# Kernel tuning notes

Measured on AMD Instinct MI355X. Metric: run time of the kernel, lower is better.

Reference implementation:

```python
import jax, jax.numpy as jnp
import numpy as np

HIDDEN = 2048
HEAD_DIM = 128
GROUPS = 8
HEADS = HIDDEN // HEAD_DIM          # 16
HPG = HEADS // GROUPS               # heads per group = 2


def setup_inputs() -> dict:
    key = jax.random.key(0)
    ks = jax.random.split(key, 9)
    b, sl, sk = 2, 2048, 2048
    s = 0.02
    return {
        "q": jax.random.normal(ks[0], (b, sl, HIDDEN), jnp.float32),
        "k": jax.random.normal(ks[1], (b, sk, HIDDEN), jnp.float32),
        "v": jax.random.normal(ks[2], (b, sk, HIDDEN), jnp.float32),
        "Wq": jax.random.normal(ks[3], (HIDDEN, HIDDEN), jnp.float32) * s,
        "bq": jax.random.normal(ks[4], (HIDDEN,), jnp.float32) * s,
        "Wk": jax.random.normal(ks[5], (HIDDEN, HEAD_DIM * GROUPS), jnp.float32) * s,
        "bk": jax.random.normal(ks[6], (HEAD_DIM * GROUPS,), jnp.float32) * s,
        "Wv": jax.random.normal(ks[7], (HIDDEN, HEAD_DIM * GROUPS), jnp.float32) * s,
        "bv": jax.random.normal(ks[8], (HEAD_DIM * GROUPS,), jnp.float32) * s,
    }


def reference(q, k, v, Wq, bq, Wk, bk, Wv, bv):
    b, sl, _ = q.shape
    sk = k.shape[1]
    qp = q @ Wq + bq                                   # [b, sl, hidden]
    kp = k @ Wk + bk                                   # [b, sk, G*d]
    vp = v @ Wv + bv                                   # [b, sk, G*d]
    # head h = g*HPG + j uses group g, matching torch repeat_interleave on dim=1
    qh = qp.reshape(b, sl, GROUPS, HPG, HEAD_DIM).transpose(0, 2, 3, 1, 4)  # [b,G,hpg,sl,d]
    kh = kp.reshape(b, sk, GROUPS, HEAD_DIM).transpose(0, 2, 1, 3)          # [b,G,sk,d]
    vh = vp.reshape(b, sk, GROUPS, HEAD_DIM).transpose(0, 2, 1, 3)          # [b,G,sk,d]
    scale = 1.0 / jnp.sqrt(jnp.asarray(HEAD_DIM, qh.dtype))
    score = jnp.einsum("bghld,bgsd->bghls", qh, kh) * scale                 # [b,G,hpg,sl,sk]
    attn = jax.nn.softmax(score, axis=-1)
    out = jnp.einsum("bghls,bgsd->bghld", attn, vh)                         # [b,G,hpg,sl,d]
    out = out.transpose(0, 3, 1, 2, 4).reshape(b, sl, HIDDEN)
    return out
```

## Files before the change

### kernel.cpp

```cpp
#include <hip/hip_runtime.h>

typedef unsigned short u16;
typedef short v8s __attribute__((ext_vector_type(8)));
typedef float v4f __attribute__((ext_vector_type(4)));
typedef float v16f __attribute__((ext_vector_type(16)));

typedef __attribute__((address_space(3))) u16* lptr_t;
typedef const __attribute__((address_space(1))) void* gptr_t;

__device__ __forceinline__ u16 f2b(float f) {
  unsigned int u = __float_as_uint(f);
  u += 0x7fff + ((u >> 16) & 1);
  return (u16)(u >> 16);
}

__global__ __launch_bounds__(256) void conv3_bf16(const float* __restrict__ q,
                                                  const float* __restrict__ k,
                                                  const float* __restrict__ v,
                                                  u16* __restrict__ qd,
                                                  u16* __restrict__ kd,
                                                  u16* __restrict__ vd) {
  int blk = blockIdx.x;
  const float* s; u16* d;
  if (blk < 4096)      { s = q; d = qd; }
  else if (blk < 8192) { s = k; d = kd; blk -= 4096; }
  else                 { s = v; d = vd; blk -= 8192; }
  int i = (blk * 256 + threadIdx.x) * 8;
  float4 a = *(const float4*)&s[i];
  float4 b = *(const float4*)&s[i + 4];
  union { uint4 v4; u16 u[8]; } p;
  p.u[0] = f2b(a.x); p.u[1] = f2b(a.y); p.u[2] = f2b(a.z); p.u[3] = f2b(a.w);
  p.u[4] = f2b(b.x); p.u[5] = f2b(b.y); p.u[6] = f2b(b.z); p.u[7] = f2b(b.w);
  *(uint4*)&d[i] = p.v4;
}

__global__ __launch_bounds__(256) void transp3_w(const float* __restrict__ Wq,
                                                 const float* __restrict__ Wk,
                                                 const float* __restrict__ Wv,
                                                 u16* __restrict__ wt) {
  __shared__ u16 tile[64][65];
  int blk = blockIdx.x;
  const float* W; int N; u16* dst;
  if (blk < 1024)      { W = Wq; N = 2048; dst = wt; }
  else if (blk < 1536) { W = Wk; N = 1024; dst = wt + (size_t)2048 * 2048; blk -= 1024; }
  else                 { W = Wv; N = 1024; dst = wt + (size_t)3072 * 2048; blk -= 1536; }
  const int k0 = (blk & 31) * 64;
  const int n0 = (blk >> 5) * 64;
  const int t = threadIdx.x;
#pragma unroll
  for (int i = 0; i < 2; ++i) {
    int chunk = i * 256 + t;
    int kr = chunk >> 3;
    int nc = (chunk & 7) * 8;
    float4 a = *(const float4*)&W[(size_t)(k0 + kr) * N + n0 + nc];
    float4 b = *(const float4*)&W[(size_t)(k0 + kr) * N + n0 + nc + 4];
    tile[kr][nc + 0] = f2b(a.x); tile[kr][nc + 1] = f2b(a.y);
    tile[kr][nc + 2] = f2b(a.z); tile[kr][nc + 3] = f2b(a.w);
    tile[kr][nc + 4] = f2b(b.x); tile[kr][nc + 5] = f2b(b.y);
    tile[kr][nc + 6] = f2b(b.z); tile[kr][nc + 7] = f2b(b.w);
  }
  __syncthreads();
#pragma unroll
  for (int i = 0; i < 2; ++i) {
    int chunk = i * 256 + t;
    int nr = chunk >> 3;
    int kc = (chunk & 7) * 8;
    union { uint4 v; u16 u[8]; } cv;
#pragma unroll
    for (int j = 0; j < 8; ++j) cv.u[j] = tile[kc + j][nr];
    *(uint4*)&dst[(size_t)(n0 + nr) * 2048 + k0 + kc] = cv.v;
  }
}

__global__ __launch_bounds__(512, 2) void qkv_gemm8(const u16* __restrict__ qbf,
                                                    const u16* __restrict__ kbf,
                                                    const u16* __restrict__ vbf,
                                                    const u16* __restrict__ wt_all,
                                                    const float* __restrict__ bq,
                                                    const float* __restrict__ bk,
                                                    const float* __restrict__ bv,
                                                    u16* __restrict__ qp,
                                                    u16* __restrict__ kp,
                                                    u16* __restrict__ vpt) {
  __shared__ __align__(16) u16 A_sh[2][16384];
  __shared__ __align__(16) u16 B_sh[2][16384];

  const int bid = blockIdx.x;
  const int wg = (bid & 7) * 32 + (bid >> 3);
  const int m0 = (wg >> 4) * 256;
  const int n0 = (wg & 15) * 256;

  const int t = threadIdx.x;
  const int w = t >> 6, lane = t & 63;
  const int quad = lane >> 4, l16 = lane & 15;
  const int wr = w >> 2, wc = w & 3;

  const u16* Abase; const float* bias; int region, nloc0;
  if (n0 < 2048)      { Abase = qbf; bias = bq; region = 0; nloc0 = n0; }
  else if (n0 < 3072) { Abase = kbf; bias = bk; region = 1; nloc0 = n0 - 2048; }
  else                { Abase = vbf; bias = bv; region = 2; nloc0 = n0 - 3072; }

  const u16* GA = Abase + (size_t)m0 * 2048;
  const u16* GB = wt_all + (size_t)n0 * 2048;

  int offA[2][2], ldsA[2][2], offB[2][2], ldsB[2][2];
#pragma unroll
  for (int s_ = 0; s_ < 2; ++s_)
#pragma unroll
    for (int j = 0; j < 2; ++j) {
      int r0a = j * 128 + s_ * 64 + w * 8;
      int ra = r0a + (lane >> 3);
      offA[s_][j] = ra * 2048 + (((lane & 7) ^ (((ra >> 2) & 1) << 1)) << 3);
      ldsA[s_][j] = r0a * 64 + lane * 8;
      int r0b = j * 128 + s_ * 32 + (w >> 2) * 64 + (w & 3) * 8;
      int rb = r0b + (lane >> 3);
      offB[s_][j] = rb * 2048 + (((lane & 7) ^ (((rb >> 2) & 1) << 1)) << 3);
      ldsB[s_][j] = r0b * 64 + lane * 8;
    }

  int colK[2];
#pragma unroll
  for (int kk = 0; kk < 2; ++kk)
    colK[kk] = (kk * 32 + quad * 8) ^ (((l16 >> 2) & 1) << 4);

#define ST_A(BUF, KEL, S_)                                                              \
  do {                                                                                  \
    _Pragma("unroll") for (int j_ = 0; j_ < 2; ++j_) {                                  \
      const u16* g_ = GA + (KEL) + offA[S_][j_];                                        \
      lptr_t l_ = (lptr_t)&A_sh[BUF][ldsA[S_][j_]];                                     \
      __builtin_amdgcn_global_load_lds((gptr_t)g_,                                      \
                                       (__attribute__((address_space(3))) void*)l_,     \
                                       16, 0, 0);                                       \
    }                                                                                   \
  } while (0)

#define ST_B(BUF, KEL, S_)                                                              \
  do {                                                                                  \
    _Pragma("unroll") for (int j_ = 0; j_ < 2; ++j_) {                                  \
      const u16* g_ = GB + (KEL) + offB[S_][j_];                                        \
      lptr_t l_ = (lptr_t)&B_sh[BUF][ldsB[S_][j_]];                                     \
      __builtin_amdgcn_global_load_lds((gptr_t)g_,                                      \
                                       (__attribute__((address_space(3))) void*)l_,     \
                                       16, 0, 0);                                       \
    }                                                                                   \
  } while (0)

#define RD_A(BUF, MS)                                                                   \
  do {                                                                                  \
    const int rb_ = wr * 128 + (MS) * 64;                                               \
    _Pragma("unroll") for (int m_ = 0; m_ < 4; ++m_)                                    \
    _Pragma("unroll") for (int kk_ = 0; kk_ < 2; ++kk_)                                 \
      a[m_][kk_] = *(const v8s*)&A_sh[BUF][(rb_ + m_ * 16 + l16) * 64 + colK[kk_]];     \
  } while (0)

#define RD_B(BUF, NS)                                                                   \
  do {                                                                                  \
    const int rb_ = wc * 64 + (NS) * 32;                                                \
    _Pragma("unroll") for (int n_ = 0; n_ < 2; ++n_)                                    \
    _Pragma("unroll") for (int kk_ = 0; kk_ < 2; ++kk_)                                 \
      b[n_][kk_] = *(const v8s*)&B_sh[BUF][(rb_ + n_ * 16 + l16) * 64 + colK[kk_]];     \
  } while (0)

#define MM(MS, NS)                                                                      \
  do {                                                                                  \
    __builtin_amdgcn_s_setprio(1);                                                      \
    _Pragma("unroll") for (int kk_ = 0; kk_ < 2; ++kk_)                                 \
    _Pragma("unroll") for (int m_ = 0; m_ < 4; ++m_)                                    \
    _Pragma("unroll") for (int n_ = 0; n_ < 2; ++n_)                                    \
      acc[(MS) * 4 + m_][(NS) * 2 + n_] = __builtin_amdgcn_mfma_f32_16x16x32_bf16(      \
          a[m_][kk_], b[n_][kk_], acc[(MS) * 4 + m_][(NS) * 2 + n_], 0, 0, 0);          \
    __builtin_amdgcn_s_setprio(0);                                                      \
  } while (0)

#define PHASE_MID()                                                                     \
  do {                                                                                  \
    asm volatile("" ::: "memory");                                                      \
    __builtin_amdgcn_s_barrier();                                                       \
    asm volatile("s_waitcnt lgkmcnt(0)" ::: "memory");                                  \
    __builtin_amdgcn_sched_barrier(0);                                                  \
  } while (0)

#define PHASE_END()                                                                     \
  do {                                                                                  \
    asm volatile("" ::: "memory");                                                      \
    __builtin_amdgcn_s_barrier();                                                       \
    __builtin_amdgcn_sched_barrier(0);                                                  \
  } while (0)

#define PHASE_END_V()                                                                   \
  do {                                                                                  \
    asm volatile("s_waitcnt vmcnt(6)" ::: "memory");                                    \
    __builtin_amdgcn_s_barrier();                                                       \
    __builtin_amdgcn_sched_barrier(0);                                                  \
  } while (0)

  v4f acc[8][4] = {};
  v8s a[4][2], b[2][2];

  ST_A(0, 0, 0); ST_B(0, 0, 0); ST_A(0, 0, 1); ST_B(0, 0, 1);
  ST_B(1, 64, 0); ST_A(1, 64, 1); ST_B(1, 64, 1);
  asm volatile("s_waitcnt vmcnt(6)" ::: "memory");
  __builtin_amdgcn_s_barrier();
  __builtin_amdgcn_sched_barrier(0);

  for (int it = 0; it < 16; ++it) {
    const int k1 = (2 * it + 1) * 64;
    const int k2 = ((2 * it + 2) & 31) * 64;
    const int k3 = ((2 * it + 3) & 31) * 64;
    RD_A(0, 0); RD_B(0, 0); ST_A(1, k1, 0); PHASE_MID(); MM(0, 0); PHASE_END();
    RD_A(0, 1);             ST_B(0, k2, 0); PHASE_MID(); MM(1, 0); PHASE_END();
    RD_B(0, 1);             ST_A(0, k2, 1); PHASE_MID(); MM(1, 1); PHASE_END();
    RD_A(0, 0);             ST_B(0, k2, 1); PHASE_MID(); MM(0, 1); PHASE_END_V();
    RD_A(1, 0); RD_B(1, 0); ST_A(0, k2, 0); PHASE_MID(); MM(0, 0); PHASE_END();
    RD_A(1, 1);             ST_B(1, k3, 0); PHASE_MID(); MM(1, 0); PHASE_END();
    RD_B(1, 1);             ST_A(1, k3, 1); PHASE_MID(); MM(1, 1); PHASE_END();
    RD_A(1, 0);             ST_B(1, k3, 1); PHASE_MID(); MM(0, 1); PHASE_END_V();
  }

#undef ST_A
#undef ST_B
#undef RD_A
#undef RD_B
#undef MM
#undef PHASE_MID
#undef PHASE_END
#undef PHASE_END_V

#pragma unroll
  for (int n = 0; n < 4; ++n) {
    int nl = nloc0 + wc * 64 + n * 16 + l16;
    float bvl = bias[nl];
    if (region == 0) {
#pragma unroll
      for (int m = 0; m < 8; ++m)
#pragma unroll
        for (int r = 0; r < 4; ++r) {
          int mg = m0 + wr * 128 + m * 16 + quad * 4 + r;
          qp[(size_t)mg * 2048 + nl] = f2b((acc[m][n][r] + bvl) * 0.08838834764831845f);
        }
    } else if (region == 1) {
#pragma unroll
      for (int m = 0; m < 8; ++m)
#pragma unroll
        for (int r = 0; r < 4; ++r) {
          int mg = m0 + wr * 128 + m * 16 + quad * 4 + r;
          kp[(size_t)mg * 1024 + nl] = f2b(acc[m][n][r] + bvl);
        }
    } else {
      int g = nl >> 7, d = nl & 127;
#pragma unroll
      for (int m = 0; m < 8; ++m) {
        int mb = m0 + wr * 128 + m * 16 + quad * 4;
        int bb = mb >> 11, s = mb & 2047;
        ushort4 pk;
        pk.x = f2b(acc[m][n][0] + bvl);
        pk.y = f2b(acc[m][n][1] + bvl);
        pk.z = f2b(acc[m][n][2] + bvl);
        pk.w = f2b(acc[m][n][3] + bvl);
        *(ushort4*)&vpt[(((size_t)bb * 8 + g) * 128 + d) * 2048 + s] = pk;
      }
    }
  }
}

__global__ __launch_bounds__(256, 2) void gqa_attn2(const u16* __restrict__ qp,
                                                    const u16* __restrict__ kp,
                                                    const u16* __restrict__ vpt,
                                                    float* __restrict__ out) {
  __shared__ __align__(16) u16 K_sh[2][64 * 128];
  __shared__ __align__(16) u16 V_sh[2][128 * 64];

  const int qtile = blockIdx.x;
  const int head = blockIdx.y;
  const int batch = blockIdx.z;
  const int g = head >> 1;
  const int q0 = qtile * 128;

  const u16* qpb = qp + (size_t)batch * 2048 * 2048;
  const u16* kpb = kp + (size_t)batch * 2048 * 1024;
  const u16* vptb = vpt + (size_t)batch * 8 * 128 * 2048;
  float* outb = out + (size_t)batch * 2048 * 2048;

  const int t = threadIdx.x;
  const int wave = t >> 6, lane = t & 63;
  const int l = lane & 31, h = lane >> 5;

  v8s qf[8];
  {
    const u16* qrow = &qpb[(size_t)(q0 + wave * 32 + l) * 2048 + head * 128];
#pragma unroll
    for (int ks = 0; ks < 8; ++ks)
      qf[ks] = *(const v8s*)&qrow[ks * 16 + h * 8];
  }

  int colK[8];
#pragma unroll
  for (int ks = 0; ks < 8; ++ks) colK[ks] = ((2 * ks + h) ^ (l & 7)) * 8;

  int koff[4], voff[4];
#pragma unroll
  for (int i = 0; i < 4; ++i) {
    int krow = wave * 16 + i * 4 + (lane >> 4);
    int kg = (lane & 15) ^ (krow & 7);
    koff[i] = krow * 1024 + g * 128 + kg * 8;
    int vrow = wave * 32 + i * 8 + (lane >> 3);
    int vg = (lane & 7) ^ (vrow & 7);
    voff[i] = (g * 128 + vrow) * 2048 + vg * 8;
  }

#define STAGE_KV(BUF, S0)                                                               \
  do {                                                                                  \
    _Pragma("unroll") for (int i_ = 0; i_ < 4; ++i_) {                                  \
      const u16* gk_ = kpb + (size_t)(S0) * 1024 + koff[i_];                            \
      lptr_t lk_ = (lptr_t)&K_sh[BUF][(wave * 16 + i_ * 4) * 128] + lane * 8;           \
      __builtin_amdgcn_global_load_lds((gptr_t)gk_,                                     \
                                       (__attribute__((address_space(3))) void*)lk_,    \
                                       16, 0, 0);                                       \
      const u16* gv_ = vptb + voff[i_] + (S0);                                          \
      lptr_t lv_ = (lptr_t)&V_sh[BUF][(wave * 32 + i_ * 8) * 64] + lane * 8;            \
      __builtin_amdgcn_global_load_lds((gptr_t)gv_,                                     \
                                       (__attribute__((address_space(3))) void*)lv_,    \
                                       16, 0, 0);                                       \
    }                                                                                   \
  } while (0)

  v16f o_acc[4] = {};
  float rs = 0.0f;

  STAGE_KV(0, 0);
  __syncthreads();

  int cur = 0;
  for (int sc = 0; sc < 32; ++sc) {
    if (sc < 31) STAGE_KV(cur ^ 1, (sc + 1) * 64);

    v16f sacc[2] = {};
    __builtin_amdgcn_s_setprio(1);
#pragma unroll
    for (int kb = 0; kb < 2; ++kb)
#pragma unroll
      for (int ks = 0; ks < 8; ++ks) {
        v8s kf = *(const v8s*)&K_sh[cur][(kb * 32 + l) * 128 + colK[ks]];
        sacc[kb] = __builtin_amdgcn_mfma_f32_32x32x16_bf16(kf, qf[ks], sacc[kb], 0, 0, 0);
      }
    __builtin_amdgcn_s_setprio(0);

    unsigned int wv[16];
#pragma unroll
    for (int kb = 0; kb < 2; ++kb)
#pragma unroll
      for (int p = 0; p < 8; ++p) {
        float e0 = __expf(sacc[kb][2 * p]);
        float e1 = __expf(sacc[kb][2 * p + 1]);
        rs += e0 + e1;
        asm("v_cvt_pk_bf16_f32 %0, %1, %2" : "=v"(wv[kb * 8 + p]) : "v"(e0), "v"(e1));
      }

    v8s pa[4];
#pragma unroll
    for (int j = 0; j < 4; ++j) {
      unsigned int a = wv[j * 4 + 0], c = wv[j * 4 + 1];
      unsigned int b = wv[j * 4 + 2], d = wv[j * 4 + 3];
      asm("v_permlane32_swap_b32 %0, %1" : "+v"(a), "+v"(b));
      asm("v_permlane32_swap_b32 %0, %1" : "+v"(c), "+v"(d));
      union { unsigned int u[4]; v8s s; } pk;
      pk.u[0] = a; pk.u[1] = c; pk.u[2] = b; pk.u[3] = d;
      pa[j] = pk.s;
    }

    __builtin_amdgcn_s_setprio(1);
#pragma unroll
    for (int j = 0; j < 4; ++j)
#pragma unroll
      for (int db = 0; db < 4; ++db) {
        v8s vf = *(const v8s*)&V_sh[cur][(db * 32 + l) * 64 + colK[j]];
        o_acc[db] = __builtin_amdgcn_mfma_f32_32x32x16_bf16(pa[j], vf, o_acc[db], 0, 0, 0);
      }
    __builtin_amdgcn_s_setprio(0);

    __syncthreads();
    cur ^= 1;
  }

  float rst = rs + __shfl_xor(rs, 32, 64);
  float inv = 1.0f / rst;
#pragma unroll
  for (int r = 0; r < 16; ++r) {
    int qpat = (r & 3) + 8 * (r >> 2) + 4 * h;
    float invq = __shfl(inv, qpat, 64);
    int qrow = q0 + wave * 32 + qpat;
    float* orow = &outb[(size_t)qrow * 2048 + head * 128 + l];
#pragma unroll
    for (int db = 0; db < 4; ++db)
      orow[db * 32] = o_acc[db][r] * invq;
  }
#undef STAGE_KV
}

extern "C" void kernel_launch(void* const* d_in, const int* in_sizes, int n_in,
                              void* d_out, int out_size, void* d_ws, size_t ws_size,
                              hipStream_t stream) {
  const float* q  = (const float*)d_in[0];
  const float* k  = (const float*)d_in[1];
  const float* v  = (const float*)d_in[2];
  const float* Wq = (const float*)d_in[3];
  const float* bq = (const float*)d_in[4];
  const float* Wk = (const float*)d_in[5];
  const float* bk = (const float*)d_in[6];
  const float* Wv = (const float*)d_in[7];
  const float* bv = (const float*)d_in[8];
  float* out = (float*)d_out;
  char* ws = (char*)d_ws;

  u16* qbf    = (u16*)(ws + 0);
  u16* kbf    = (u16*)(ws + 16777216);
  u16* vbf    = (u16*)(ws + 33554432);
  u16* wt_all = (u16*)(ws + 50331648);
  u16* qp     = (u16*)(ws + 67108864);
  u16* kp     = (u16*)(ws + 83886080);
  u16* vpt    = (u16*)(ws + 92274688);

  conv3_bf16<<<12288, 256, 0, stream>>>(q, k, v, qbf, kbf, vbf);
  transp3_w<<<2048, 256, 0, stream>>>(Wq, Wk, Wv, wt_all);
  qkv_gemm8<<<256, 512, 0, stream>>>(qbf, kbf, vbf, wt_all,
                                     bq, bk, bv, qp, kp, vpt);
  gqa_attn2<<<dim3(16, 16, 2), 256, 0, stream>>>(qp, kp, vpt, out);
}
```

Measured before the change: 338.0 us.

## Use full XOR-8 LDS swizzle and double-buffer A fragments to skip re-read

Changes the LDS swizzle for the projection GEMM from a single-bit XOR to a full 3-bit XOR of the 16-byte chunk index with the row. This is meant to remove bank conflicts on the ds_read of A and B fragments. It also keeps two register sets for the A fragments, so the fourth phase of each half-iteration reuses the already loaded first-half A tile instead of reading it from LDS again. The cost is higher VGPR pressure from the extra fragment array, which could reduce occupancy or cause spills.

After: 320.3 us. -5.2%, faster.

```diff
diff --git a/kernel.cpp b/kernel.cpp
--- a/kernel.cpp
+++ b/kernel.cpp
@@ -110,18 +110,18 @@
     for (int j = 0; j < 2; ++j) {
       int r0a = j * 128 + s_ * 64 + w * 8;
       int ra = r0a + (lane >> 3);
-      offA[s_][j] = ra * 2048 + (((lane & 7) ^ (((ra >> 2) & 1) << 1)) << 3);
+      offA[s_][j] = ra * 2048 + (((lane & 7) ^ (ra & 7)) << 3);
       ldsA[s_][j] = r0a * 64 + lane * 8;
       int r0b = j * 128 + s_ * 32 + (w >> 2) * 64 + (w & 3) * 8;
       int rb = r0b + (lane >> 3);
-      offB[s_][j] = rb * 2048 + (((lane & 7) ^ (((rb >> 2) & 1) << 1)) << 3);
+      offB[s_][j] = rb * 2048 + (((lane & 7) ^ (rb & 7)) << 3);
       ldsB[s_][j] = r0b * 64 + lane * 8;
     }
 
-  int colK[2];
+  int colR[2];
 #pragma unroll
   for (int kk = 0; kk < 2; ++kk)
-    colK[kk] = (kk * 32 + quad * 8) ^ (((l16 >> 2) & 1) << 4);
+    colR[kk] = ((kk * 4 + quad) ^ (l16 & 7)) << 3;
 
 #define ST_A(BUF, KEL, S_)                                                              \
   do {                                                                                  \
@@ -145,12 +145,12 @@
     }                                                                                   \
   } while (0)
 
-#define RD_A(BUF, MS)                                                                   \
+#define RD_A(BUF, MS, DST)                                                              \
   do {                                                                                  \
     const int rb_ = wr * 128 + (MS) * 64;                                               \
     _Pragma("unroll") for (int m_ = 0; m_ < 4; ++m_)                                    \
     _Pragma("unroll") for (int kk_ = 0; kk_ < 2; ++kk_)                                 \
-      a[m_][kk_] = *(const v8s*)&A_sh[BUF][(rb_ + m_ * 16 + l16) * 64 + colK[kk_]];     \
+      DST[m_][kk_] = *(const v8s*)&A_sh[BUF][(rb_ + m_ * 16 + l16) * 64 + colR[kk_]];   \
   } while (0)
 
 #define RD_B(BUF, NS)                                                                   \
@@ -158,17 +158,17 @@
     const int rb_ = wc * 64 + (NS) * 32;                                                \
     _Pragma("unroll") for (int n_ = 0; n_ < 2; ++n_)                                    \
     _Pragma("unroll") for (int kk_ = 0; kk_ < 2; ++kk_)                                 \
-      b[n_][kk_] = *(const v8s*)&B_sh[BUF][(rb_ + n_ * 16 + l16) * 64 + colK[kk_]];     \
-  } while (0)
-
-#define MM(MS, NS)                                                                      \
+      b[n_][kk_] = *(const v8s*)&B_sh[BUF][(rb_ + n_ * 16 + l16) * 64 + colR[kk_]];     \
+  } while (0)
+
+#define MM(AR, MS, NS)                                                                  \
   do {                                                                                  \
     __builtin_amdgcn_s_setprio(1);                                                      \
     _Pragma("unroll") for (int kk_ = 0; kk_ < 2; ++kk_)                                 \
     _Pragma("unroll") for (int m_ = 0; m_ < 4; ++m_)                                    \
     _Pragma("unroll") for (int n_ = 0; n_ < 2; ++n_)                                    \
       acc[(MS) * 4 + m_][(NS) * 2 + n_] = __builtin_amdgcn_mfma_f32_16x16x32_bf16(      \
-          a[m_][kk_], b[n_][kk_], acc[(MS) * 4 + m_][(NS) * 2 + n_], 0, 0, 0);          \
+          AR[m_][kk_], b[n_][kk_], acc[(MS) * 4 + m_][(NS) * 2 + n_], 0, 0, 0);         \
     __builtin_amdgcn_s_setprio(0);                                                      \
   } while (0)
 
@@ -195,7 +195,7 @@
   } while (0)
 
   v4f acc[8][4] = {};
-  v8s a[4][2], b[2][2];
+  v8s a0[4][2], a1[4][2], b[2][2];
 
   ST_A(0, 0, 0); ST_B(0, 0, 0); ST_A(0, 0, 1); ST_B(0, 0, 1);
   ST_B(1, 64, 0); ST_A(1, 64, 1); ST_B(1, 64, 1);
@@ -207,14 +207,14 @@
     const int k1 = (2 * it + 1) * 64;
     const int k2 = ((2 * it + 2) & 31) * 64;
     const int k3 = ((2 * it + 3) & 31) * 64;
-    RD_A(0, 0); RD_B(0, 0); ST_A(1, k1, 0); PHASE_MID(); MM(0, 0); PHASE_END();
-    RD_A(0, 1);             ST_B(0, k2, 0); PHASE_MID(); MM(1, 0); PHASE_END();
-    RD_B(0, 1);             ST_A(0, k2, 1); PHASE_MID(); MM(1, 1); PHASE_END();
-    RD_A(0, 0);             ST_B(0, k2, 1); PHASE_MID(); MM(0, 1); PHASE_END_V();
-    RD_A(1, 0); RD_B(1, 0); ST_A(0, k2, 0); PHASE_MID(); MM(0, 0); PHASE_END();
-    RD_A(1, 1);             ST_B(1, k3, 0); PHASE_MID(); MM(1, 0); PHASE_END();
-    RD_B(1, 1);             ST_A(1, k3, 1); PHASE_MID(); MM(1, 1); PHASE_END();
-    RD_A(1, 0);             ST_B(1, k3, 1); PHASE_MID(); MM(0, 1); PHASE_END_V();
+    RD_A(0, 0, a0); RD_B(0, 0); ST_A(1, k1, 0); PHASE_MID(); MM(a0, 0, 0); PHASE_END();
+    RD_A(0, 1, a1);             ST_B(0, k2, 0); PHASE_MID(); MM(a1, 1, 0); PHASE_END();
+    RD_B(0, 1);                 ST_A(0, k2, 1); PHASE_MID(); MM(a1, 1, 1); PHASE_END();
+                                ST_B(0, k2, 1); PHASE_MID(); MM(a0, 0, 1); PHASE_END_V();
+    RD_A(1, 0, a0); RD_B(1, 0); ST_A(0, k2, 0); PHASE_MID(); MM(a0, 0, 0); PHASE_END();
+    RD_A(1, 1, a1);             ST_B(1, k3, 0); PHASE_MID(); MM(a1, 1, 0); PHASE_END();
+    RD_B(1, 1);                 ST_A(1, k3, 1); PHASE_MID(); MM(a1, 1, 1); PHASE_END();
+                                ST_B(1, k3, 1); PHASE_MID(); MM(a0, 0, 1); PHASE_END_V();
   }
 
 #undef ST_A
```
